# Kernel tuning notes

Measured on AMD Instinct MI355X. Metric: run time of the kernel, lower is better.

## Reference

```python
import jax, jax.numpy as jnp
import numpy as np

NUM_HEADS = 16
NEG_INF = -9000000000000000.0


def setup_inputs() -> dict:
    key = jax.random.key(0)
    ks = jax.random.split(key, 4)
    B, S, D = 2, 2048, 1024
    x = jax.random.normal(ks[0], (B, S, D), dtype=jnp.float32)
    mask = jax.random.randint(ks[1], (1, 1, S, S), 0, 2, dtype=jnp.int32)
    # xavier-uniform-ish init scaled down for stability
    w_qkv = jax.random.normal(ks[2], (3 * D, D), dtype=jnp.float32) * (1.0 / np.sqrt(D))
    b_qkv = jnp.zeros((3 * D,), dtype=jnp.float32)
    w_o = jax.random.normal(ks[3], (D, D), dtype=jnp.float32) * (1.0 / np.sqrt(D))
    b_o = jnp.zeros((D,), dtype=jnp.float32)
    return {"x": x, "mask": mask, "w_qkv": w_qkv, "b_qkv": b_qkv, "w_o": w_o, "b_o": b_o}


def reference(x, mask, w_qkv, b_qkv, w_o, b_o):
    B, S, D = x.shape
    H = NUM_HEADS
    hd = D // H
    # qkv projection: torch Linear is x @ W.T + b
    qkv = x @ w_qkv.T + b_qkv                      # [B, S, 3D]
    qkv = qkv.reshape(B, S, H, 3 * hd).transpose(0, 2, 1, 3)  # [B, H, S, 3hd]
    q, k, v = jnp.split(qkv, 3, axis=-1)           # each [B, H, S, hd]
    scale = 1.0 / np.sqrt(hd).astype(np.float32)
    logits = jnp.einsum("bhqd,bhkd->bhqk", q, k) * scale  # [B, H, S, S]
    logits = jnp.where(mask == 0, NEG_INF, logits)
    attn = jax.nn.softmax(logits, axis=-1)
    ctx = jnp.einsum("bhqk,bhkd->bhqd", attn, v)   # [B, H, S, hd]
    ctx = ctx.transpose(0, 2, 1, 3).reshape(B, S, D)
    return ctx @ w_o.T + b_o
```

## Files before the change

### kernel.cpp

```cpp
#include <hip/hip_runtime.h>

typedef __attribute__((ext_vector_type(8))) short short8;
typedef __attribute__((ext_vector_type(4))) float f32x4;

#define MFMA16(a, b, c) __builtin_amdgcn_mfma_f32_16x16x32_bf16(a, b, c, 0, 0, 0)

#define BATCH 2
#define SEQ 2048
#define DMODEL 1024
#define NHEADS 16
#define HDIM 64
#define MROWS (BATCH * SEQ)
#define N_QKV (3 * DMODEL)

#define QSCALE 0.1803368801111184f

#define GLDS16(gp, lp)                                                       \
  __builtin_amdgcn_global_load_lds(                                          \
      (const __attribute__((address_space(1))) void*)(gp),                   \
      (__attribute__((address_space(3))) void*)(lp), 16, 0, 0)

static __device__ __forceinline__ unsigned short f2bf(float f) {
  unsigned int u = __float_as_uint(f);
  u = (u + 0x7fff + ((u >> 16) & 1)) >> 16;
  return (unsigned short)u;
}

static __device__ __forceinline__ unsigned int pk2bf(float lo, float hi) {
  unsigned int r;
  asm("v_cvt_pk_bf16_f32 %0, %1, %2" : "=v"(r) : "v"(lo), "v"(hi));
  return r;
}

__global__ void cvt_kernel(const float* __restrict__ in,
                           unsigned short* __restrict__ out, int n4) {
  int i = blockIdx.x * blockDim.x + threadIdx.x;
  if (i >= n4) return;
  f32x4 v = ((const f32x4*)in)[i];
  ushort4 o;
  o.x = f2bf(v[0]); o.y = f2bf(v[1]); o.z = f2bf(v[2]); o.w = f2bf(v[3]);
  ((ushort4*)out)[i] = o;
}

__global__ void mask_to_bits(const int* __restrict__ mask,
                             unsigned int* __restrict__ bits) {
  int i = blockIdx.x * blockDim.x + threadIdx.x;
  const int* p = mask + (size_t)i * 32;
  unsigned int v = 0;
#pragma unroll
  for (int b = 0; b < 32; ++b) v |= (p[b] != 0 ? 1u : 0u) << b;
  bits[i] = v;
}

template <int EPI>
__global__ __launch_bounds__(256) void gemm_bt(
    const unsigned short* __restrict__ A, const unsigned short* __restrict__ Bm,
    const float* __restrict__ bias, int Kdim, int Ndim,
    unsigned short* __restrict__ qb, unsigned short* __restrict__ kb,
    unsigned short* __restrict__ vtb, float* __restrict__ Cout) {
  __shared__ __align__(16) unsigned short lA[128 * 40];
  __shared__ __align__(16) unsigned short lB[128 * 40];

  int t = threadIdx.x;
  int m0 = blockIdx.y * 128, n0 = blockIdx.x * 128;
  int w = t >> 6, lane = t & 63, quad = lane >> 4, l16 = lane & 15;
  int wm = (w >> 1) * 64, wn = (w & 1) * 64;

  f32x4 acc[4][4];
#pragma unroll
  for (int i = 0; i < 4; ++i)
#pragma unroll
    for (int j = 0; j < 4; ++j) acc[i][j] = (f32x4){0.f, 0.f, 0.f, 0.f};

  int nK = Kdim >> 5;
  for (int kk = 0; kk < nK; ++kk) {
    __syncthreads();
#pragma unroll
    for (int c = 0; c < 2; ++c) {
      int id = t + c * 256;
      int row = id >> 2, c8 = (id & 3) << 3;
      *(uint4*)&lA[row * 40 + c8] =
          *(const uint4*)&A[(size_t)(m0 + row) * Kdim + (kk << 5) + c8];
      *(uint4*)&lB[row * 40 + c8] =
          *(const uint4*)&Bm[(size_t)(n0 + row) * Kdim + (kk << 5) + c8];
    }
    __syncthreads();
    short8 af[4], bfr[4];
#pragma unroll
    for (int i = 0; i < 4; ++i)
      af[i] = *(const short8*)&lA[(wm + i * 16 + l16) * 40 + quad * 8];
#pragma unroll
    for (int j = 0; j < 4; ++j)
      bfr[j] = *(const short8*)&lB[(wn + j * 16 + l16) * 40 + quad * 8];
#pragma unroll
    for (int i = 0; i < 4; ++i)
#pragma unroll
      for (int j = 0; j < 4; ++j) acc[i][j] = MFMA16(af[i], bfr[j], acc[i][j]);
  }

#pragma unroll
  for (int j = 0; j < 4; ++j) {
    int n = n0 + wn + j * 16 + l16;
    float bs = bias[n];
#pragma unroll
    for (int i = 0; i < 4; ++i) {
#pragma unroll
      for (int r = 0; r < 4; ++r) {
        int m = m0 + wm + i * 16 + quad * 4 + r;
        float v = acc[i][j][r] + bs;
        if (EPI == 0) {
          int b = m >> 11, s = m & 2047;
          int h = n / 192, rr = n % 192;
          int bh = (b << 4) + h;
          if (rr < 64)
            qb[((size_t)bh * SEQ + s) * HDIM + rr] = f2bf(v * QSCALE);
          else if (rr < 128)
            kb[((size_t)bh * SEQ + s) * HDIM + (rr - 64)] = f2bf(v);
          else
            vtb[((size_t)bh * HDIM + (rr - 128)) * SEQ + s] = f2bf(v);
        } else {
          Cout[(size_t)m * Ndim + n] = v;
        }
      }
    }
  }
}

__global__ __launch_bounds__(512, 4) void attn_kernel(
    const unsigned short* __restrict__ qbuf, const unsigned short* __restrict__ kbuf,
    const unsigned short* __restrict__ vtbuf, const unsigned int* __restrict__ mbits,
    unsigned short* __restrict__ ctx) {
  __shared__ __align__(16) unsigned short lK[2][64 * 64];
  __shared__ __align__(16) unsigned short lV[2][64 * 64];
  __shared__ __align__(16) unsigned short lP[128 * 64];

  int qt = blockIdx.x, bh = blockIdx.y;
  int q0 = qt * 128;
  const unsigned short* Q = qbuf + (size_t)bh * SEQ * HDIM;
  const unsigned short* K = kbuf + (size_t)bh * SEQ * HDIM;
  const unsigned short* VT = vtbuf + (size_t)bh * HDIM * SEQ;

  int t = threadIdx.x;
  int w = t >> 6, lane = t & 63, quad = lane >> 4, l16 = lane & 15;
  int swz = (l16 & 7) << 4;

  int qrow = q0 + w * 16 + l16;
  short8 qf0 = *(const short8*)&Q[(size_t)qrow * HDIM + quad * 8];
  short8 qf1 = *(const short8*)&Q[(size_t)qrow * HDIM + 32 + quad * 8];

  f32x4 o[4];
#pragma unroll
  for (int jt = 0; jt < 4; ++jt) o[jt] = (f32x4){0.f, 0.f, 0.f, 0.f};
  float mi = -INFINITY, li = 0.f;

  int srow = w * 8 + (lane >> 3);
  int scol = ((lane & 7) ^ (srow & 7)) << 3;
  const unsigned short* gK = K + (size_t)srow * HDIM + scol;
  const unsigned short* gV = VT + (size_t)srow * SEQ + scol;

  GLDS16(gK, &lK[0][w * 512]);
  GLDS16(gV, &lV[0][w * 512]);
  gK += 64 * HDIM;
  gV += 64;

  const unsigned int* mrow = mbits + (size_t)qrow * 64;
  unsigned short* lPr = &lP[(w * 16 + l16) * 64];

  for (int it = 0; it < SEQ / 64; ++it) {
    __syncthreads();
    if (it + 1 < SEQ / 64) {
      GLDS16(gK, &lK[(it + 1) & 1][w * 512]);
      GLDS16(gV, &lV[(it + 1) & 1][w * 512]);
      gK += 64 * HDIM;
      gV += 64;
    }
    const unsigned short* cK = lK[it & 1];
    const unsigned short* cV = lV[it & 1];

    f32x4 s[4];
#pragma unroll
    for (int j = 0; j < 4; ++j) {
      const char* kr = (const char*)&cK[(j * 16 + l16) * 64];
      short8 ka = *(const short8*)(kr + ((quad * 16) ^ swz));
      short8 kc = *(const short8*)(kr + ((64 + quad * 16) ^ swz));
      f32x4 z = (f32x4){0.f, 0.f, 0.f, 0.f};
      z = MFMA16(ka, qf0, z);
      z = MFMA16(kc, qf1, z);
      s[j] = z;
    }

    uint2 mw = *(const uint2*)&mrow[it * 2];
    unsigned int ma = mw.x >> (quad * 4);
    unsigned int mb = mw.y >> (quad * 4);
#pragma unroll
    for (int j = 0; j < 4; ++j) {
      unsigned int sel = (j < 2) ? ma : mb;
      int sh = (j & 1) << 4;
#pragma unroll
      for (int r = 0; r < 4; ++r)
        s[j][r] = (sel & (1u << (sh + r))) ? s[j][r] : -1e30f;
    }

    float mx = fmaxf(fmaxf(s[0][0], s[0][1]), fmaxf(s[0][2], s[0][3]));
#pragma unroll
    for (int j = 1; j < 4; ++j)
      mx = fmaxf(mx, fmaxf(fmaxf(s[j][0], s[j][1]), fmaxf(s[j][2], s[j][3])));
    mx = fmaxf(mx, __shfl_xor(mx, 16));
    mx = fmaxf(mx, __shfl_xor(mx, 32));
    float mn = fmaxf(mi, mx);
    float al = exp2f(mi - mn);
    float rs = 0.f;
#pragma unroll
    for (int j = 0; j < 4; ++j)
#pragma unroll
      for (int r = 0; r < 4; ++r) {
        float p = exp2f(s[j][r] - mn);
        s[j][r] = p;
        rs += p;
      }
    rs += __shfl_xor(rs, 16);
    rs += __shfl_xor(rs, 32);
    li = li * al + rs;
    mi = mn;
#pragma unroll
    for (int jt = 0; jt < 4; ++jt)
#pragma unroll
      for (int r = 0; r < 4; ++r) o[jt][r] *= al;

#pragma unroll
    for (int j = 0; j < 4; ++j) {
      uint2 u;
      u.x = pk2bf(s[j][0], s[j][1]);
      u.y = pk2bf(s[j][2], s[j][3]);
      *(uint2*)((char*)lPr + ((j * 32 + quad * 8) ^ swz)) = u;
    }

#pragma unroll
    for (int kh = 0; kh < 2; ++kh) {
      short8 pf = *(const short8*)((const char*)lPr + ((kh * 64 + quad * 16) ^ swz));
#pragma unroll
      for (int jt = 0; jt < 4; ++jt) {
        const char* vr = (const char*)&cV[(jt * 16 + l16) * 64];
        short8 vf = *(const short8*)(vr + ((kh * 64 + quad * 16) ^ swz));
        o[jt] = MFMA16(vf, pf, o[jt]);
      }
    }
  }

  float inv = 1.f / li;
  int b = bh >> 4, h = bh & 15;
  unsigned short* crow = ctx + ((size_t)(b * SEQ + qrow)) * DMODEL + h * HDIM;
#pragma unroll
  for (int jt = 0; jt < 4; ++jt) {
    uint2 u;
    u.x = pk2bf(o[jt][0] * inv, o[jt][1] * inv);
    u.y = pk2bf(o[jt][2] * inv, o[jt][3] * inv);
    *(uint2*)&crow[jt * 16 + quad * 4] = u;
  }
}

extern "C" void kernel_launch(void* const* d_in, const int* in_sizes, int n_in,
                              void* d_out, int out_size, void* d_ws, size_t ws_size,
                              hipStream_t stream) {
  const float* x = (const float*)d_in[0];
  const int* mask = (const int*)d_in[1];
  const float* w_qkv = (const float*)d_in[2];
  const float* b_qkv = (const float*)d_in[3];
  const float* w_o = (const float*)d_in[4];
  const float* b_o = (const float*)d_in[5];
  float* out = (float*)d_out;

  char* ws = (char*)d_ws;
  unsigned short* xb = (unsigned short*)(ws);
  unsigned short* wqkvb = (unsigned short*)(ws + (8ull << 20));
  unsigned short* wob = (unsigned short*)(ws + (14ull << 20));
  unsigned short* qb = (unsigned short*)(ws + (16ull << 20));
  unsigned short* kb = (unsigned short*)(ws + (24ull << 20));
  unsigned short* vtb = (unsigned short*)(ws + (32ull << 20));
  unsigned short* ctx = (unsigned short*)(ws + (40ull << 20));
  unsigned int* mbits = (unsigned int*)(ws + (48ull << 20));

  cvt_kernel<<<4096, 256, 0, stream>>>(x, xb, (MROWS * DMODEL) / 4);
  cvt_kernel<<<3072, 256, 0, stream>>>(w_qkv, wqkvb, (N_QKV * DMODEL) / 4);
  cvt_kernel<<<1024, 256, 0, stream>>>(w_o, wob, (DMODEL * DMODEL) / 4);
  mask_to_bits<<<512, 256, 0, stream>>>(mask, mbits);

  gemm_bt<0><<<dim3(N_QKV / 128, MROWS / 128), 256, 0, stream>>>(
      xb, wqkvb, b_qkv, DMODEL, N_QKV, qb, kb, vtb, nullptr);

  attn_kernel<<<dim3(SEQ / 128, BATCH * NHEADS), 512, 0, stream>>>(
      qb, kb, vtb, mbits, ctx);

  gemm_bt<1><<<dim3(DMODEL / 128, MROWS / 128), 256, 0, stream>>>(
      ctx, wob, b_o, DMODEL, DMODEL, nullptr, nullptr, nullptr, out);
}
```

Before: 255.6 us.

## Shrink attention blocks to 64 queries, add lazy rescale, XCD swizzle, setprio

Attention blocks go from 512 threads covering 128 query rows to 256 threads covering 64 rows, so each wave now stages two K/V rows per tile and the grid doubles. Block indices are remapped so that neighbouring query tiles of the same head fall on the same XCD, aiming for better L2 reuse of K/V. The online softmax now rescales only when the running max grows by more than a threshold, and MFMA sections are wrapped in s_setprio. The risks are more K/V traffic per query row, and the unnormalised exponentials can grow large because the starting max is zero instead of minus infinity.

```diff
diff --git a/kernel.cpp b/kernel.cpp
--- a/kernel.cpp
+++ b/kernel.cpp
@@ -126,16 +126,18 @@
   }
 }
 
-__global__ __launch_bounds__(512, 4) void attn_kernel(
+__global__ __launch_bounds__(256, 4) void attn_kernel(
     const unsigned short* __restrict__ qbuf, const unsigned short* __restrict__ kbuf,
     const unsigned short* __restrict__ vtbuf, const unsigned int* __restrict__ mbits,
     unsigned short* __restrict__ ctx) {
   __shared__ __align__(16) unsigned short lK[2][64 * 64];
   __shared__ __align__(16) unsigned short lV[2][64 * 64];
-  __shared__ __align__(16) unsigned short lP[128 * 64];
-
-  int qt = blockIdx.x, bh = blockIdx.y;
-  int q0 = qt * 128;
+  __shared__ __align__(16) unsigned short lP[64 * 64];
+
+  int lin = blockIdx.y * gridDim.x + blockIdx.x;
+  int slin = (lin & 7) * 128 + (lin >> 3);
+  int qt = slin & 31, bh = slin >> 5;
+  int q0 = qt * 64;
   const unsigned short* Q = qbuf + (size_t)bh * SEQ * HDIM;
   const unsigned short* K = kbuf + (size_t)bh * SEQ * HDIM;
   const unsigned short* VT = vtbuf + (size_t)bh * HDIM * SEQ;
@@ -151,15 +153,21 @@
   f32x4 o[4];
 #pragma unroll
   for (int jt = 0; jt < 4; ++jt) o[jt] = (f32x4){0.f, 0.f, 0.f, 0.f};
-  float mi = -INFINITY, li = 0.f;
-
-  int srow = w * 8 + (lane >> 3);
-  int scol = ((lane & 7) ^ (srow & 7)) << 3;
-  const unsigned short* gK = K + (size_t)srow * HDIM + scol;
-  const unsigned short* gV = VT + (size_t)srow * SEQ + scol;
-
-  GLDS16(gK, &lK[0][w * 512]);
-  GLDS16(gV, &lV[0][w * 512]);
+  float mi = 0.f, li = 0.f;
+
+  int scol = ((lane & 7) ^ (lane >> 3)) << 3;
+  const unsigned short* gK = K + (size_t)(w * 8 + (lane >> 3)) * HDIM + scol;
+  const unsigned short* gV = VT + (size_t)(w * 8 + (lane >> 3)) * SEQ + scol;
+
+#define STAGE_KV(buf)                                            \
+  do {                                                           \
+    GLDS16(gK, &lK[buf][(w * 8) * 64]);                          \
+    GLDS16(gK + 32 * HDIM, &lK[buf][(32 + w * 8) * 64]);         \
+    GLDS16(gV, &lV[buf][(w * 8) * 64]);                          \
+    GLDS16(gV + 32 * SEQ, &lV[buf][(32 + w * 8) * 64]);          \
+  } while (0)
+
+  STAGE_KV(0);
   gK += 64 * HDIM;
   gV += 64;
 
@@ -169,15 +177,17 @@
   for (int it = 0; it < SEQ / 64; ++it) {
     __syncthreads();
     if (it + 1 < SEQ / 64) {
-      GLDS16(gK, &lK[(it + 1) & 1][w * 512]);
-      GLDS16(gV, &lV[(it + 1) & 1][w * 512]);
+      STAGE_KV((it + 1) & 1);
       gK += 64 * HDIM;
       gV += 64;
     }
     const unsigned short* cK = lK[it & 1];
     const unsigned short* cV = lV[it & 1];
 
+    uint2 mw = *(const uint2*)&mrow[it * 2];
+
     f32x4 s[4];
+    __builtin_amdgcn_s_setprio(1);
 #pragma unroll
     for (int j = 0; j < 4; ++j) {
       const char* kr = (const char*)&cK[(j * 16 + l16) * 64];
@@ -188,8 +198,8 @@
       z = MFMA16(kc, qf1, z);
       s[j] = z;
     }
-
-    uint2 mw = *(const uint2*)&mrow[it * 2];
+    __builtin_amdgcn_s_setprio(0);
+
     unsigned int ma = mw.x >> (quad * 4);
     unsigned int mb = mw.y >> (quad * 4);
 #pragma unroll
@@ -201,31 +211,42 @@
         s[j][r] = (sel & (1u << (sh + r))) ? s[j][r] : -1e30f;
     }
 
-    float mx = fmaxf(fmaxf(s[0][0], s[0][1]), fmaxf(s[0][2], s[0][3]));
-#pragma unroll
-    for (int j = 1; j < 4; ++j)
-      mx = fmaxf(mx, fmaxf(fmaxf(s[j][0], s[j][1]), fmaxf(s[j][2], s[j][3])));
+    float x0 = fmaxf(fmaxf(s[0][0], s[0][1]), fmaxf(s[0][2], s[0][3]));
+    float x1 = fmaxf(fmaxf(s[1][0], s[1][1]), fmaxf(s[1][2], s[1][3]));
+    float x2 = fmaxf(fmaxf(s[2][0], s[2][1]), fmaxf(s[2][2], s[2][3]));
+    float x3 = fmaxf(fmaxf(s[3][0], s[3][1]), fmaxf(s[3][2], s[3][3]));
+    float mx = fmaxf(fmaxf(x0, x1), fmaxf(x2, x3));
     mx = fmaxf(mx, __shfl_xor(mx, 16));
     mx = fmaxf(mx, __shfl_xor(mx, 32));
-    float mn = fmaxf(mi, mx);
-    float al = exp2f(mi - mn);
-    float rs = 0.f;
+
 #pragma unroll
     for (int j = 0; j < 4; ++j)
 #pragma unroll
-      for (int r = 0; r < 4; ++r) {
-        float p = exp2f(s[j][r] - mn);
-        s[j][r] = p;
-        rs += p;
-      }
+      for (int r = 0; r < 4; ++r) s[j][r] = exp2f(s[j][r] - mi);
+    float r0 = (s[0][0] + s[0][1]) + (s[0][2] + s[0][3]);
+    float r1 = (s[1][0] + s[1][1]) + (s[1][2] + s[1][3]);
+    float r2 = (s[2][0] + s[2][1]) + (s[2][2] + s[2][3]);
+    float r3 = (s[3][0] + s[3][1]) + (s[3][2] + s[3][3]);
+    float rs = (r0 + r1) + (r2 + r3);
+
+    if (!__all(mx <= mi + 5.f)) {
+      float mn = fmaxf(mi, mx);
+      float al = exp2f(mi - mn);
+#pragma unroll
+      for (int j = 0; j < 4; ++j)
+#pragma unroll
+        for (int r = 0; r < 4; ++r) s[j][r] *= al;
+      rs *= al;
+#pragma unroll
+      for (int jt = 0; jt < 4; ++jt)
+#pragma unroll
+        for (int r = 0; r < 4; ++r) o[jt][r] *= al;
+      li *= al;
+      mi = mn;
+    }
     rs += __shfl_xor(rs, 16);
     rs += __shfl_xor(rs, 32);
-    li = li * al + rs;
-    mi = mn;
-#pragma unroll
-    for (int jt = 0; jt < 4; ++jt)
-#pragma unroll
-      for (int r = 0; r < 4; ++r) o[jt][r] *= al;
+    li += rs;
 
 #pragma unroll
     for (int j = 0; j < 4; ++j) {
@@ -235,6 +256,7 @@
       *(uint2*)((char*)lPr + ((j * 32 + quad * 8) ^ swz)) = u;
     }
 
+    __builtin_amdgcn_s_setprio(1);
 #pragma unroll
     for (int kh = 0; kh < 2; ++kh) {
       short8 pf = *(const short8*)((const char*)lPr + ((kh * 64 + quad * 16) ^ swz));
@@ -245,6 +267,7 @@
         o[jt] = MFMA16(vf, pf, o[jt]);
       }
     }
+    __builtin_amdgcn_s_setprio(0);
   }
 
   float inv = 1.f / li;
@@ -288,7 +311,7 @@
   gemm_bt<0><<<dim3(N_QKV / 128, MROWS / 128), 256, 0, stream>>>(
       xb, wqkvb, b_qkv, DMODEL, N_QKV, qb, kb, vtb, nullptr);
 
-  attn_kernel<<<dim3(SEQ / 128, BATCH * NHEADS), 512, 0, stream>>>(
+  attn_kernel<<<dim3(SEQ / 64, BATCH * NHEADS), 256, 0, stream>>>(
       qb, kb, vtb, mbits, ctx);
 
   gemm_bt<1><<<dim3(DMODEL / 128, MROWS / 128), 256, 0, stream>>>(
```

After: 252.9 us. Within noise of the previous version (-1.1%).
